# Optimization experiments

Measured on AMD Instinct MI355X. Metric: run time of the kernel, lower is better.

Reference implementation:

```python
import jax, jax.numpy as jnp
import numpy as np

B, S, D, H = 2, 2048, 1024, 16
HD = D // H  # head dim = 64


def setup_inputs() -> dict:
    key0 = jax.random.key(0)
    ks = jax.random.split(key0, 12)
    scale = 1.0 / np.sqrt(D)
    inp = {
        "query": jax.random.normal(ks[0], (B, S, D), jnp.float32),
        "key": jax.random.normal(ks[1], (B, S, D), jnp.float32),
        "value": jax.random.normal(ks[2], (B, S, D), jnp.float32),
        "mask": jax.random.randint(ks[3], (B, S), 0, 2, jnp.int32),
        "Wq": jax.random.normal(ks[4], (D, D), jnp.float32) * scale,
        "bq": jnp.zeros((D,), jnp.float32),
        "Wk": jax.random.normal(ks[5], (D, D), jnp.float32) * scale,
        "bk": jnp.zeros((D,), jnp.float32),
        "Wv": jax.random.normal(ks[6], (D, D), jnp.float32) * scale,
        "bv": jnp.zeros((D,), jnp.float32),
        "Wo": jax.random.normal(ks[7], (D, D), jnp.float32) * scale,
        "bo": jnp.zeros((D,), jnp.float32),
    }
    return inp


def _split_heads(x):  # (B,S,D) -> (B,H,S,HD)
    Bb, Ss, Dd = x.shape
    return x.reshape(Bb, Ss, H, HD).transpose(0, 2, 1, 3)


def reference(query, key, value, mask, Wq, bq, Wk, bk, Wv, bv, Wo, bo):
    # Linear projections (torch Linear: x @ W.T + b), split into heads.
    q = _split_heads(query @ Wq.T + bq)
    k = _split_heads(key @ Wk.T + bk)
    v = _split_heads(value @ Wv.T + bv)
    # Scaled dot-product scores: (B,H,S,S); NOTE: original divides by sqrt(head_dim).
    scores = jnp.einsum("bhqd,bhkd->bhqk", q, k) / np.sqrt(HD).astype(np.float32)
    # mask (B,S) masks KEY positions; broadcast over heads and query positions.
    scores = jnp.where(mask[:, None, None, :] == 0, jnp.float32(-1e9), scores)
    attn = jax.nn.softmax(scores, axis=-1)
    # Dropout is identity in eval mode.
    x = jnp.einsum("bhqk,bhkd->bhqd", attn, v)  # (B,H,S,HD)
    x = x.transpose(0, 2, 1, 3).reshape(query.shape[0], query.shape[1], D)
    return x @ Wo.T + bo
```

## Files before the change

### kernel.cpp

```cpp
#include <hip/hip_runtime.h>
#include <hip/hip_bf16.h>
#include <hip/hip_fp16.h>

#define BB 2
#define SS 2048
#define DD 1024
#define HH 16
#define HD 64
#define MM (BB * SS)

typedef __attribute__((ext_vector_type(8))) _Float16 half8;
typedef __attribute__((ext_vector_type(4))) float f32x4;
typedef __attribute__((ext_vector_type(4))) short short4v;

static __device__ __forceinline__ short f2h(float f) {
    _Float16 h = (_Float16)f;
    return __builtin_bit_cast(short, h);
}

static __device__ __forceinline__ unsigned pk2(float a, float b) {
    auto h = __builtin_amdgcn_cvt_pkrtz(a, b);
    return __builtin_bit_cast(unsigned, h);
}

static __device__ __forceinline__ float fexp2(float x) {
    return __builtin_amdgcn_exp2f(x);
}

static __device__ __forceinline__ void gload16(const void* g, void* l) {
    __builtin_amdgcn_global_load_lds(
        (const __attribute__((address_space(1))) unsigned*)g,
        (__attribute__((address_space(3))) unsigned*)l, 16, 0, 0);
}

#define SC2E 0.18033688011112042f

__global__ __launch_bounds__(256) void partition_kernel(
    const int* __restrict__ mask, int* __restrict__ cpos,
    short* __restrict__ mask16, int* __restrict__ nu)
{
    const int b = blockIdx.x;
    const int t = threadIdx.x;
    __shared__ int sc[256];
    const int* mrow = mask + b * SS;
    int loc[8];
    int cnt = 0;
    #pragma unroll
    for (int j = 0; j < 8; ++j) { loc[j] = (mrow[t * 8 + j] != 0); cnt += loc[j]; }
    sc[t] = cnt;
    __syncthreads();
    for (int off = 1; off < 256; off <<= 1) {
        const int v = sc[t];
        const int va = (t >= off) ? sc[t - off] : 0;
        __syncthreads();
        sc[t] = v + va;
        __syncthreads();
    }
    const int total = sc[255];
    if (t == 0) nu[b] = total;
    int u = sc[t] - cnt;
    #pragma unroll
    for (int j = 0; j < 8; ++j) {
        const int s = t * 8 + j;
        cpos[b * SS + s] = loc[j] ? u : (total + (s - u));
        u += loc[j];
        mask16[b * SS + s] = f2h((s < total) ? 1.0f : 0.0f);
    }
}

__global__ __launch_bounds__(256) void cvt_kernel(
    const float* __restrict__ wq, const float* __restrict__ wk,
    const float* __restrict__ wv, const float* __restrict__ wo,
    short* __restrict__ wq16, short* __restrict__ wk16,
    short* __restrict__ wv16, short* __restrict__ wo16)
{
    const int i = (blockIdx.x * 256 + threadIdx.x) * 4;
    const float* src; short* dst;
    switch (blockIdx.y) {
        case 0: src = wq; dst = wq16; break;
        case 1: src = wk; dst = wk16; break;
        case 2: src = wv; dst = wv16; break;
        default: src = wo; dst = wo16; break;
    }
    if (i >= DD * DD) return;
    const float4 f = *(const float4*)&src[i];
    short4v h;
    h.x = f2h(f.x); h.y = f2h(f.y); h.z = f2h(f.z); h.w = f2h(f.w);
    *(short4v*)&dst[i] = h;
}

template<bool AFP32>
static __device__ __forceinline__ void gemm_phase(
    const short* __restrict__ AsCur, const short* __restrict__ BsCur,
    char* AsNxt, char* BsNxt,
    const void* __restrict__ A, const short* __restrict__ W,
    int m0, int n0, int k_next, bool do_stage,
    int t, int lr, int lq, int wc,
    f32x4 acc[4][2])
{
    constexpr int WN = 32;
    constexpr int NI = 2;
    const int K = DD;

    float4 af32[4];
    if (do_stage) {
        #pragma unroll
        for (int c = 0; c < 4; ++c) {
            const int b = c * 4096 + t * 16;
            const int row = b >> 7;
            const int coff = b & 127;
            const int scoff = coff ^ ((row & 7) << 4);
            gload16((const char*)W + ((size_t)(n0 + row) * K + k_next) * 2 + scoff,
                    BsNxt + b);
        }
        #pragma unroll
        for (int c = 0; c < 2; ++c) {
            const int b = c * 4096 + t * 16;
            const int row = b >> 7;
            const int coff = b & 127;
            if constexpr (AFP32) {
                const float* ap = (const float*)A +
                    (size_t)(m0 + row) * K + k_next + (coff >> 1);
                af32[c * 2]     = *(const float4*)ap;
                af32[c * 2 + 1] = *(const float4*)(ap + 4);
            } else {
                const int scoff = coff ^ ((row & 7) << 4);
                gload16((const char*)A + ((size_t)(m0 + row) * K + k_next) * 2 + scoff,
                        AsNxt + b);
            }
        }
    }

    half8 af[4][2], bf[NI][2];
    #pragma unroll
    for (int mi = 0; mi < 4; ++mi) {
        const int row = mi * 16 + lr;
        #pragma unroll
        for (int ks = 0; ks < 2; ++ks) {
            const int col = (ks * 32 + lq * 8) ^ ((row & 7) << 3);
            af[mi][ks] = *(const half8*)&AsCur[row * 64 + col];
        }
    }
    #pragma unroll
    for (int ni = 0; ni < NI; ++ni) {
        const int row = wc * WN + ni * 16 + lr;
        #pragma unroll
        for (int ks = 0; ks < 2; ++ks) {
            const int col = (ks * 32 + lq * 8) ^ ((row & 7) << 3);
            bf[ni][ks] = *(const half8*)&BsCur[row * 64 + col];
        }
    }
    __builtin_amdgcn_s_setprio(1);
    #pragma unroll
    for (int ks = 0; ks < 2; ++ks)
        #pragma unroll
        for (int mi = 0; mi < 4; ++mi)
            #pragma unroll
            for (int ni = 0; ni < NI; ++ni)
                acc[mi][ni] = __builtin_amdgcn_mfma_f32_16x16x32_f16(
                    af[mi][ks], bf[ni][ks], acc[mi][ni], 0, 0, 0);
    __builtin_amdgcn_s_setprio(0);

    if (do_stage) {
        if constexpr (AFP32) {
            #pragma unroll
            for (int c = 0; c < 2; ++c) {
                const int b = c * 4096 + t * 16;
                const int row = b >> 7;
                const int coff = b & 127;
                uint4 pv;
                pv.x = pk2(af32[c * 2].x,     af32[c * 2].y);
                pv.y = pk2(af32[c * 2].z,     af32[c * 2].w);
                pv.z = pk2(af32[c * 2 + 1].x, af32[c * 2 + 1].y);
                pv.w = pk2(af32[c * 2 + 1].z, af32[c * 2 + 1].w);
                *(uint4*)(AsNxt + row * 128 + (coff ^ ((row & 7) << 4))) = pv;
            }
        }
    }

    __syncthreads();
}

template<bool AFP32>
__global__ __launch_bounds__(256) void gemm_f16(
    const void* __restrict__ A0, const void* __restrict__ A1, const void* __restrict__ A2,
    const short* __restrict__ W0, const short* __restrict__ W1, const short* __restrict__ W2,
    const float* __restrict__ b0, const float* __restrict__ b1, const float* __restrict__ b2,
    void* __restrict__ C0, void* __restrict__ C1, void* __restrict__ C2,
    int mode0, int mode1, int mode2,
    float os0, float os1, float os2,
    int perm0, int perm1, int perm2,
    const int* __restrict__ mask, const int* __restrict__ cpos)
{
    constexpr int TM = 64;
    constexpr int WN = 32;
    constexpr int NI = 2;

    const int gx = gridDim.x, gy = gridDim.y;
    const int total = gx * gy * gridDim.z;
    const int lin = (blockIdx.z * gy + blockIdx.y) * gx + blockIdx.x;
    const int work = (lin & 7) * (total >> 3) + (lin >> 3);
    const int z = work / (gx * gy);
    const int r0 = work % (gx * gy);
    const int bx = r0 / gy;
    const int by = r0 % gy;

    const void* A = (z == 0) ? A0 : (z == 1) ? A1 : A2;
    const short* W = (z == 0) ? W0 : (z == 1) ? W1 : W2;
    const float* bias = (z == 0) ? b0 : (z == 1) ? b1 : b2;
    void* C = (z == 0) ? C0 : (z == 1) ? C1 : C2;
    const int mode = (z == 0) ? mode0 : (z == 1) ? mode1 : mode2;
    const float os = (z == 0) ? os0 : (z == 1) ? os1 : os2;
    const int perm = (z == 0) ? perm0 : (z == 1) ? perm1 : perm2;

    __shared__ short Asw[2][TM * 64];
    __shared__ short Bsw[2][128 * 64];

    const int t = threadIdx.x;
    const int wave = t >> 6, lane = t & 63;
    const int lr = lane & 15, lq = lane >> 4;
    const int wc = wave;
    const int m0 = bx * TM, n0 = by * 128;
    const int K = DD;

    f32x4 acc[4][NI] = {};

    {
        #pragma unroll
        for (int c = 0; c < 4; ++c) {
            const int b = c * 4096 + t * 16;
            const int row = b >> 7;
            const int coff = b & 127;
            const int scoff = coff ^ ((row & 7) << 4);
            gload16((const char*)W + ((size_t)(n0 + row) * K) * 2 + scoff,
                    (char*)Bsw[0] + b);
        }
        #pragma unroll
        for (int c = 0; c < 2; ++c) {
            const int b = c * 4096 + t * 16;
            const int row = b >> 7;
            const int coff = b & 127;
            if constexpr (AFP32) {
                const float* ap = (const float*)A + (size_t)(m0 + row) * K + (coff >> 1);
                const float4 f0 = *(const float4*)ap;
                const float4 f1 = *(const float4*)(ap + 4);
                uint4 pv;
                pv.x = pk2(f0.x, f0.y);
                pv.y = pk2(f0.z, f0.w);
                pv.z = pk2(f1.x, f1.y);
                pv.w = pk2(f1.z, f1.w);
                *(uint4*)((char*)Asw[0] + row * 128 + (coff ^ ((row & 7) << 4))) = pv;
            } else {
                const int scoff = coff ^ ((row & 7) << 4);
                gload16((const char*)A + ((size_t)(m0 + row) * K) * 2 + scoff,
                        (char*)Asw[0] + b);
            }
        }
    }
    __syncthreads();

    for (int k0 = 0; k0 < K; k0 += 128) {
        gemm_phase<AFP32>(Asw[0], Bsw[0], (char*)Asw[1], (char*)Bsw[1],
                          A, W, m0, n0, k0 + 64, true,
                          t, lr, lq, wc, acc);
        gemm_phase<AFP32>(Asw[1], Bsw[1], (char*)Asw[0], (char*)Bsw[0],
                          A, W, m0, n0, k0 + 128, (k0 + 128) < K,
                          t, lr, lq, wc, acc);
    }

    if (mode == 2) {
        #pragma unroll
        for (int mi = 0; mi < 4; ++mi) {
            const int mbase = m0 + mi * 16 + lq * 4;
            const int bidx = mbase >> 11;
            const int4 mk = *(const int4*)&mask[mbase];
            const int4 cp = *(const int4*)&cpos[mbase];
            const float mmul[4] = { mk.x ? 1.0f : 0.0f, mk.y ? 1.0f : 0.0f,
                                    mk.z ? 1.0f : 0.0f, mk.w ? 1.0f : 0.0f };
            const int cpr[4] = { cp.x, cp.y, cp.z, cp.w };
            #pragma unroll
            for (int ni = 0; ni < NI; ++ni) {
                const int n = n0 + wc * WN + ni * 16 + lr;
                const int h = n >> 6, d = n & (HD - 1);
                const float bi = bias[n];
                short* cb = &((short*)C)[(((size_t)bidx * HH + h) * HD + d) * SS];
                #pragma unroll
                for (int r = 0; r < 4; ++r)
                    cb[cpr[r]] = f2h((acc[mi][ni][r] + bi) * mmul[r]);
            }
        }
    } else {
        #pragma unroll
        for (int mi = 0; mi < 4; ++mi) {
            #pragma unroll
            for (int r = 0; r < 4; ++r) {
                const int m = m0 + mi * 16 + lq * 4 + r;
                const int bidx = m >> 11;
                const int s = (mode == 1 && perm) ? cpos[m] : (m & (SS - 1));
                #pragma unroll
                for (int ni = 0; ni < NI; ++ni) {
                    const int n = n0 + wc * WN + ni * 16 + lr;
                    const float val = (acc[mi][ni][r] + bias[n]) * os;
                    if (mode == 0) {
                        ((float*)C)[(size_t)m * DD + n] = val;
                    } else {
                        const int h = n >> 6, d = n & (HD - 1);
                        ((short*)C)[(((size_t)bidx * HH + h) * SS + s) * HD + d] = f2h(val);
                    }
                }
            }
        }
    }
}

static __device__ __forceinline__ void attn_tile_body(
    const short* __restrict__ Ks, const short* __restrict__ Vts,
    char* KsN, char* VtsN,
    const char* kb, const char* vb,
    int kv_stage, bool do_stage,
    const short* __restrict__ mrow, int kv0,
    const half8 qf[2], short* Pw,
    int t, int lr, int lq,
    f32x4 o[4], f32x4& ol)
{
    if (do_stage) {
        #pragma unroll
        for (int c = 0; c < 2; ++c) {
            const int off = c * 4096 + t * 16;
            const int row = off >> 7, coff = off & 127;
            const int sw = coff ^ ((row & 7) << 4);
            gload16(kb + (size_t)(kv_stage + row) * 128 + sw, KsN + off);
            gload16(vb + (size_t)row * (SS * 2) + kv_stage * 2 + sw, VtsN + off);
        }
    }

    half8 mf[2];
    #pragma unroll
    for (int ks = 0; ks < 2; ++ks)
        mf[ks] = *(const half8*)&mrow[kv0 + ks * 32 + lq * 8];

    f32x4 sc[4] = {};
    __builtin_amdgcn_s_setprio(1);
    #pragma unroll
    for (int kt = 0; kt < 4; ++kt) {
        const int kr = kt * 16 + lr;
        #pragma unroll
        for (int ks = 0; ks < 2; ++ks) {
            half8 kf = *(const half8*)&Ks[kr * 64 + ((ks * 32 + lq * 8) ^ ((kr & 7) << 3))];
            sc[kt] = __builtin_amdgcn_mfma_f32_16x16x32_f16(kf, qf[ks], sc[kt], 0, 0, 0);
        }
    }
    __builtin_amdgcn_s_setprio(0);

    const int xsw = (lr & 7) << 3;
    #pragma unroll
    for (int kt = 0; kt < 4; ++kt) {
        const float p0 = fexp2(sc[kt][0]);
        const float p1 = fexp2(sc[kt][1]);
        const float p2 = fexp2(sc[kt][2]);
        const float p3 = fexp2(sc[kt][3]);
        const int cb = kt * 16 + lq * 4;
        uint2 pp;
        pp.x = pk2(p0, p1);
        pp.y = pk2(p2, p3);
        *(uint2*)&Pw[lr * 64 + (cb ^ xsw)] = pp;
    }

    half8 pf[2];
    #pragma unroll
    for (int ks = 0; ks < 2; ++ks)
        pf[ks] = *(const half8*)&Pw[lr * 64 + ((ks * 32 + lq * 8) ^ xsw)];
    __builtin_amdgcn_s_setprio(1);
    #pragma unroll
    for (int ks = 0; ks < 2; ++ks)
        ol = __builtin_amdgcn_mfma_f32_16x16x32_f16(pf[ks], mf[ks], ol, 0, 0, 0);
    #pragma unroll
    for (int dt = 0; dt < 4; ++dt) {
        const int dr = dt * 16 + lr;
        #pragma unroll
        for (int ks = 0; ks < 2; ++ks) {
            half8 vf = *(const half8*)&Vts[dr * 64 + ((ks * 32 + lq * 8) ^ ((dr & 7) << 3))];
            o[dt] = __builtin_amdgcn_mfma_f32_16x16x32_f16(pf[ks], vf, o[dt], 0, 0, 0);
        }
    }
    __builtin_amdgcn_s_setprio(0);

    __syncthreads();
}

__global__ __launch_bounds__(256) void attn_mfma_kernel(
    const short* __restrict__ q,
    const short* __restrict__ k,
    const short* __restrict__ vt,
    const short* __restrict__ mask16,
    const int* __restrict__ nu,
    short* __restrict__ x)
{
    const int lin = (blockIdx.z * HH + blockIdx.y) * (SS / 64) + blockIdx.x;
    const int swz = (lin & 7) * 128 + (lin >> 3);
    const int qt = swz & 31;
    const int hb = swz >> 5;
    const int h  = hb & (HH - 1);
    const int b  = hb >> 4;

    const int t = threadIdx.x;
    const int wave = t >> 6, lane = t & 63;
    const int lr = lane & 15;
    const int lq = lane >> 4;

    __shared__ short QPs[64 * 64];
    __shared__ short KsD[2][64 * 64];
    __shared__ short VtsD[2][64 * 64];

    const size_t base  = ((size_t)(b * HH + h)) * SS * HD;
    const size_t basev = ((size_t)(b * HH + h)) * HD * SS;
    const char* kb = (const char*)(k + base);
    const char* vb = (const char*)(vt + basev);

    const int limit = ((nu[b] + 63) >> 6) << 6;

    {
        const char* qb = (const char*)(q + base + (size_t)qt * 64 * HD);
        #pragma unroll
        for (int c = 0; c < 2; ++c) {
            const int off = c * 4096 + t * 16;
            const int row = off >> 7, coff = off & 127;
            const int sw = coff ^ ((row & 7) << 4);
            gload16(qb + row * 128 + sw, (char*)QPs + off);
            gload16(kb + (size_t)row * 128 + sw, (char*)KsD[0] + off);
            gload16(vb + (size_t)row * (SS * 2) + sw, (char*)VtsD[0] + off);
        }
    }
    __syncthreads();

    half8 qf[2];
    #pragma unroll
    for (int ks = 0; ks < 2; ++ks) {
        const int r = wave * 16 + lr;
        qf[ks] = *(const half8*)&QPs[r * 64 + ((ks * 32 + lq * 8) ^ ((r & 7) << 3))];
    }
    __syncthreads();

    f32x4 o[4] = {};
    f32x4 ol = {};
    const short* mrow = &mask16[b * SS];
    short* Pw = &QPs[wave * 1024];

    for (int kv0 = 0; kv0 < limit; kv0 += 128) {
        attn_tile_body(KsD[0], VtsD[0], (char*)KsD[1], (char*)VtsD[1],
                       kb, vb, kv0 + 64, (kv0 + 64) < limit,
                       mrow, kv0, qf, Pw, t, lr, lq, o, ol);
        if (kv0 + 64 < limit)
            attn_tile_body(KsD[1], VtsD[1], (char*)KsD[0], (char*)VtsD[0],
                           kb, vb, kv0 + 128, (kv0 + 128) < limit,
                           mrow, kv0 + 64, qf, Pw, t, lr, lq, o, ol);
    }

    float linv[4];
    #pragma unroll
    for (int r = 0; r < 4; ++r) linv[r] = 1.0f / ol[r];
    const int srow = qt * 64 + wave * 16;
    #pragma unroll
    for (int dt = 0; dt < 4; ++dt)
        #pragma unroll
        for (int r = 0; r < 4; ++r)
            x[((size_t)b * SS + srow + lq * 4 + r) * DD + h * HD + dt * 16 + lr] =
                f2h(o[dt][r] * linv[r]);
}

extern "C" void kernel_launch(void* const* d_in, const int* in_sizes, int n_in,
                              void* d_out, int out_size, void* d_ws, size_t ws_size,
                              hipStream_t stream) {
    const float* query = (const float*)d_in[0];
    const float* key   = (const float*)d_in[1];
    const float* value = (const float*)d_in[2];
    const int*   mask  = (const int*)d_in[3];
    const float* Wq = (const float*)d_in[4];
    const float* bq = (const float*)d_in[5];
    const float* Wk = (const float*)d_in[6];
    const float* bk = (const float*)d_in[7];
    const float* Wv = (const float*)d_in[8];
    const float* bv = (const float*)d_in[9];
    const float* Wo = (const float*)d_in[10];
    const float* bo = (const float*)d_in[11];
    float* out = (float*)d_out;

    const size_t NACT = (size_t)MM * DD;
    const size_t NW   = (size_t)DD * DD;
    short* wq16   = (short*)d_ws;
    short* wk16   = wq16 + NW;
    short* wv16   = wk16 + NW;
    short* wo16   = wv16 + NW;
    short* q_ws   = wo16 + NW;
    short* k_ws   = q_ws + NACT;
    short* vt_ws  = k_ws + NACT;
    short* mask16 = vt_ws + NACT;
    short* x16    = mask16 + BB * SS;
    int*   cpos   = (int*)(x16 + NACT);
    int*   nu     = cpos + BB * SS;

    partition_kernel<<<dim3(BB), 256, 0, stream>>>(mask, cpos, mask16, nu);

    cvt_kernel<<<dim3(NW / 4 / 256, 4), 256, 0, stream>>>(
        Wq, Wk, Wv, Wo, wq16, wk16, wv16, wo16);

    gemm_f16<true><<<dim3(MM / 64, DD / 128, 3), 256, 0, stream>>>(
        query, key, value, wq16, wk16, wv16, bq, bk, bv,
        q_ws, k_ws, vt_ws, 1, 1, 2, SC2E, 1.0f, 1.0f,
        0, 1, 1, mask, cpos);

    attn_mfma_kernel<<<dim3(SS / 64, HH, BB), 256, 0, stream>>>(
        q_ws, k_ws, vt_ws, mask16, nu, x16);

    gemm_f16<false><<<dim3(MM / 64, DD / 128, 1), 256, 0, stream>>>(
        x16, x16, x16, wo16, wo16, wo16, bo, bo, bo,
        out, out, out, 0, 0, 0, 1.0f, 1.0f, 1.0f,
        0, 0, 0, mask, cpos);
}
```

Baseline: 131.3 us.

## Gather projection input rows by inverse permutation instead of scattering outputs

```diff
diff --git a/kernel.cpp b/kernel.cpp
--- a/kernel.cpp
+++ b/kernel.cpp
@@ -36,7 +36,7 @@
 #define SC2E 0.18033688011112042f
 
 __global__ __launch_bounds__(256) void partition_kernel(
-    const int* __restrict__ mask, int* __restrict__ cpos,
+    const int* __restrict__ mask, int* __restrict__ ipos,
     short* __restrict__ mask16, int* __restrict__ nu)
 {
     const int b = blockIdx.x;
@@ -62,7 +62,8 @@
     #pragma unroll
     for (int j = 0; j < 8; ++j) {
         const int s = t * 8 + j;
-        cpos[b * SS + s] = loc[j] ? u : (total + (s - u));
+        const int cp = loc[j] ? u : (total + (s - u));
+        ipos[b * SS + cp] = b * SS + s;
         u += loc[j];
         mask16[b * SS + s] = f2h((s < total) ? 1.0f : 0.0f);
     }
@@ -93,7 +94,9 @@
 static __device__ __forceinline__ void gemm_phase(
     const short* __restrict__ AsCur, const short* __restrict__ BsCur,
     char* AsNxt, char* BsNxt,
-    const void* __restrict__ A, const short* __restrict__ W,
+    const float* rp0, const float* rp1,
+    const short* __restrict__ A16,
+    const short* __restrict__ W,
     int m0, int n0, int k_next, bool do_stage,
     int t, int lr, int lq, int wc,
     f32x4 acc[4][2])
@@ -113,19 +116,19 @@
             gload16((const char*)W + ((size_t)(n0 + row) * K + k_next) * 2 + scoff,
                     BsNxt + b);
         }
-        #pragma unroll
-        for (int c = 0; c < 2; ++c) {
-            const int b = c * 4096 + t * 16;
-            const int row = b >> 7;
-            const int coff = b & 127;
-            if constexpr (AFP32) {
-                const float* ap = (const float*)A +
-                    (size_t)(m0 + row) * K + k_next + (coff >> 1);
-                af32[c * 2]     = *(const float4*)ap;
-                af32[c * 2 + 1] = *(const float4*)(ap + 4);
-            } else {
+        if constexpr (AFP32) {
+            af32[0] = *(const float4*)(rp0 + k_next);
+            af32[1] = *(const float4*)(rp0 + k_next + 4);
+            af32[2] = *(const float4*)(rp1 + k_next);
+            af32[3] = *(const float4*)(rp1 + k_next + 4);
+        } else {
+            #pragma unroll
+            for (int c = 0; c < 2; ++c) {
+                const int b = c * 4096 + t * 16;
+                const int row = b >> 7;
+                const int coff = b & 127;
                 const int scoff = coff ^ ((row & 7) << 4);
-                gload16((const char*)A + ((size_t)(m0 + row) * K + k_next) * 2 + scoff,
+                gload16((const char*)A16 + ((size_t)(m0 + row) * K + k_next) * 2 + scoff,
                         AsNxt + b);
             }
         }
@@ -189,8 +192,8 @@
     void* __restrict__ C0, void* __restrict__ C1, void* __restrict__ C2,
     int mode0, int mode1, int mode2,
     float os0, float os1, float os2,
-    int perm0, int perm1, int perm2,
-    const int* __restrict__ mask, const int* __restrict__ cpos)
+    int g0, int g1, int g2,
+    const int* __restrict__ ipos, const int* __restrict__ nu)
 {
     constexpr int TM = 64;
     constexpr int WN = 32;
@@ -211,7 +214,7 @@
     void* C = (z == 0) ? C0 : (z == 1) ? C1 : C2;
     const int mode = (z == 0) ? mode0 : (z == 1) ? mode1 : mode2;
     const float os = (z == 0) ? os0 : (z == 1) ? os1 : os2;
-    const int perm = (z == 0) ? perm0 : (z == 1) ? perm1 : perm2;
+    const int g = (z == 0) ? g0 : (z == 1) ? g1 : g2;
 
     __shared__ short Asw[2][TM * 64];
     __shared__ short Bsw[2][128 * 64];
@@ -222,6 +225,18 @@
     const int wc = wave;
     const int m0 = bx * TM, n0 = by * 128;
     const int K = DD;
+
+    const int arow0 = (t * 16) >> 7;
+    const int arow1 = 32 + arow0;
+    const int acoffE = ((t * 16) & 127) >> 1;
+    const float* rp0 = nullptr;
+    const float* rp1 = nullptr;
+    if constexpr (AFP32) {
+        int fr0 = m0 + arow0, fr1 = m0 + arow1;
+        if (g) { fr0 = ipos[fr0]; fr1 = ipos[fr1]; }
+        rp0 = (const float*)A + (size_t)fr0 * DD + acoffE;
+        rp1 = (const float*)A + (size_t)fr1 * DD + acoffE;
+    }
 
     f32x4 acc[4][NI] = {};
 
@@ -235,22 +250,30 @@
             gload16((const char*)W + ((size_t)(n0 + row) * K) * 2 + scoff,
                     (char*)Bsw[0] + b);
         }
-        #pragma unroll
-        for (int c = 0; c < 2; ++c) {
-            const int b = c * 4096 + t * 16;
-            const int row = b >> 7;
-            const int coff = b & 127;
-            if constexpr (AFP32) {
-                const float* ap = (const float*)A + (size_t)(m0 + row) * K + (coff >> 1);
-                const float4 f0 = *(const float4*)ap;
-                const float4 f1 = *(const float4*)(ap + 4);
+        if constexpr (AFP32) {
+            float4 af32[4];
+            af32[0] = *(const float4*)(rp0);
+            af32[1] = *(const float4*)(rp0 + 4);
+            af32[2] = *(const float4*)(rp1);
+            af32[3] = *(const float4*)(rp1 + 4);
+            #pragma unroll
+            for (int c = 0; c < 2; ++c) {
+                const int b = c * 4096 + t * 16;
+                const int row = b >> 7;
+                const int coff = b & 127;
                 uint4 pv;
-                pv.x = pk2(f0.x, f0.y);
-                pv.y = pk2(f0.z, f0.w);
-                pv.z = pk2(f1.x, f1.y);
-                pv.w = pk2(f1.z, f1.w);
+                pv.x = pk2(af32[c * 2].x,     af32[c * 2].y);
+                pv.y = pk2(af32[c * 2].z,     af32[c * 2].w);
+                pv.z = pk2(af32[c * 2 + 1].x, af32[c * 2 + 1].y);
+                pv.w = pk2(af32[c * 2 + 1].z, af32[c * 2 + 1].w);
                 *(uint4*)((char*)Asw[0] + row * 128 + (coff ^ ((row & 7) << 4))) = pv;
-            } else {
+            }
+        } else {
+            #pragma unroll
+            for (int c = 0; c < 2; ++c) {
+                const int b = c * 4096 + t * 16;
+                const int row = b >> 7;
+                const int coff = b & 127;
                 const int scoff = coff ^ ((row & 7) << 4);
                 gload16((const char*)A + ((size_t)(m0 + row) * K) * 2 + scoff,
                         (char*)Asw[0] + b);
@@ -261,32 +284,34 @@
 
     for (int k0 = 0; k0 < K; k0 += 128) {
         gemm_phase<AFP32>(Asw[0], Bsw[0], (char*)Asw[1], (char*)Bsw[1],
-                          A, W, m0, n0, k0 + 64, true,
+                          rp0, rp1, (const short*)A, W, m0, n0, k0 + 64, true,
                           t, lr, lq, wc, acc);
         gemm_phase<AFP32>(Asw[1], Bsw[1], (char*)Asw[0], (char*)Bsw[0],
-                          A, W, m0, n0, k0 + 128, (k0 + 128) < K,
-                          t, lr, lq, wc, acc);
+                          rp0, rp1, (const short*)A, W, m0, n0, k0 + 128,
+                          (k0 + 128) < K, t, lr, lq, wc, acc);
     }
 
     if (mode == 2) {
         #pragma unroll
         for (int mi = 0; mi < 4; ++mi) {
-            const int mbase = m0 + mi * 16 + lq * 4;
-            const int bidx = mbase >> 11;
-            const int4 mk = *(const int4*)&mask[mbase];
-            const int4 cp = *(const int4*)&cpos[mbase];
-            const float mmul[4] = { mk.x ? 1.0f : 0.0f, mk.y ? 1.0f : 0.0f,
-                                    mk.z ? 1.0f : 0.0f, mk.w ? 1.0f : 0.0f };
-            const int cpr[4] = { cp.x, cp.y, cp.z, cp.w };
+            const int m = m0 + mi * 16 + lq * 4;
+            const int bidx = m >> 11;
+            const int s = m & (SS - 1);
+            const int nub = nu[bidx];
+            float mmul[4];
+            #pragma unroll
+            for (int r = 0; r < 4; ++r) mmul[r] = (s + r < nub) ? 1.0f : 0.0f;
             #pragma unroll
             for (int ni = 0; ni < NI; ++ni) {
                 const int n = n0 + wc * WN + ni * 16 + lr;
                 const int h = n >> 6, d = n & (HD - 1);
                 const float bi = bias[n];
-                short* cb = &((short*)C)[(((size_t)bidx * HH + h) * HD + d) * SS];
-                #pragma unroll
-                for (int r = 0; r < 4; ++r)
-                    cb[cpr[r]] = f2h((acc[mi][ni][r] + bi) * mmul[r]);
+                short4v pv;
+                pv.x = f2h((acc[mi][ni][0] + bi) * mmul[0]);
+                pv.y = f2h((acc[mi][ni][1] + bi) * mmul[1]);
+                pv.z = f2h((acc[mi][ni][2] + bi) * mmul[2]);
+                pv.w = f2h((acc[mi][ni][3] + bi) * mmul[3]);
+                *(short4v*)&((short*)C)[(((size_t)bidx * HH + h) * HD + d) * SS + s] = pv;
             }
         }
     } else {
@@ -296,7 +321,7 @@
             for (int r = 0; r < 4; ++r) {
                 const int m = m0 + mi * 16 + lq * 4 + r;
                 const int bidx = m >> 11;
-                const int s = (mode == 1 && perm) ? cpos[m] : (m & (SS - 1));
+                const int s = m & (SS - 1);
                 #pragma unroll
                 for (int ni = 0; ni < NI; ++ni) {
                     const int n = n0 + wc * WN + ni * 16 + lr;
@@ -496,10 +521,10 @@
     short* vt_ws  = k_ws + NACT;
     short* mask16 = vt_ws + NACT;
     short* x16    = mask16 + BB * SS;
-    int*   cpos   = (int*)(x16 + NACT);
-    int*   nu     = cpos + BB * SS;
-
-    partition_kernel<<<dim3(BB), 256, 0, stream>>>(mask, cpos, mask16, nu);
+    int*   ipos   = (int*)(x16 + NACT);
+    int*   nu     = ipos + BB * SS;
+
+    partition_kernel<<<dim3(BB), 256, 0, stream>>>(mask, ipos, mask16, nu);
 
     cvt_kernel<<<dim3(NW / 4 / 256, 4), 256, 0, stream>>>(
         Wq, Wk, Wv, Wo, wq16, wk16, wv16, wo16);
@@ -507,7 +532,7 @@
     gemm_f16<true><<<dim3(MM / 64, DD / 128, 3), 256, 0, stream>>>(
         query, key, value, wq16, wk16, wv16, bq, bk, bv,
         q_ws, k_ws, vt_ws, 1, 1, 2, SC2E, 1.0f, 1.0f,
-        0, 1, 1, mask, cpos);
+        0, 1, 1, ipos, nu);
 
     attn_mfma_kernel<<<dim3(SS / 64, HH, BB), 256, 0, stream>>>(
         q_ws, k_ws, vt_ws, mask16, nu, x16);
@@ -515,5 +540,5 @@
     gemm_f16<false><<<dim3(MM / 64, DD / 128, 1), 256, 0, stream>>>(
         x16, x16, x16, wo16, wo16, wo16, bo, bo, bo,
         out, out, out, 0, 0, 0, 1.0f, 1.0f, 1.0f,
-        0, 0, 0, mask, cpos);
-}
+        0, 0, 0, ipos, nu);
+}
```

Measured after the change: 115.8 us. -11.8%, faster.
